# Kernel optimization log

Measured on AMD Instinct MI355X. Metric: run time of the kernel, lower is better.

The kernel has to match this reference:

```python
import jax, jax.numpy as jnp
import numpy as np

N = 100000      # nodes
E = 1600000     # edges (before self-loops)
FIN = 128       # in_channels
HID = 16        # hidden_channels
H = 8           # heads (layer 1)
OUT = 64        # out_channels
LN_EPS = 1e-5


def setup_inputs() -> dict:
    key = jax.random.key(0)
    ks = jax.random.split(key, 24)
    def p(i, shape):
        return jax.random.normal(ks[i], shape, dtype=jnp.float32) * 0.05
    return {
        "x": jax.random.normal(ks[0], (N, FIN), dtype=jnp.float32),
        "edge_index": jax.random.randint(ks[1], (2, E), 0, N, dtype=jnp.int32),
        # GATv2 layer 1: in -> H*HID, concat
        "Wl1": p(2, (FIN, H * HID)), "bl1": p(3, (H * HID,)),
        "Wr1": p(4, (FIN, H * HID)), "br1": p(5, (H * HID,)),
        "att1": p(6, (H, HID)), "bias1": p(7, (H * HID,)),
        # GATv2 layer 2: H*HID -> HID, heads=1
        "Wl2": p(8, (H * HID, HID)), "bl2": p(9, (HID,)),
        "Wr2": p(10, (H * HID, HID)), "br2": p(11, (HID,)),
        "att2": p(12, (1, HID)), "bias2": p(13, (HID,)),
        # LayerNorms
        "ln1_g": jnp.ones((H * HID,), jnp.float32), "ln1_b": jnp.zeros((H * HID,), jnp.float32),
        "ln2_g": jnp.ones((HID,), jnp.float32), "ln2_b": jnp.zeros((HID,), jnp.float32),
        # residual / skip / output linears
        "res1_W": p(14, (FIN, H * HID)), "res1_b": p(15, (H * HID,)),
        "res2_W": p(16, (H * HID, HID)), "res2_b": p(17, (HID,)),
        "skip_W": p(18, (H * HID, HID)), "skip_b": p(19, (HID,)),
        "out_W": p(20, (HID, OUT)), "out_b": p(21, (OUT,)),
    }


def _layernorm(x, g, b):
    mu = jnp.mean(x, axis=-1, keepdims=True)
    var = jnp.mean((x - mu) ** 2, axis=-1, keepdims=True)
    return (x - mu) * jax.lax.rsqrt(var + LN_EPS) * g + b


def _gatv2(x, src, dst, Wl, bl, Wr, br, att, bias, concat):
    # PyG GATv2Conv (share_weights=False, eval mode): message from src j to dst i
    Hh, C = att.shape
    n = x.shape[0]
    xl = (x @ Wl + bl).reshape(n, Hh, C)   # source-side transform
    xr = (x @ Wr + br).reshape(n, Hh, C)   # target-side transform
    m = xl[src] + xr[dst]                  # [E, H, C]
    e = jax.nn.leaky_relu(m, 0.2)
    alpha = jnp.einsum('ehc,hc->eh', e, att)          # [E, H]
    amax = jax.ops.segment_max(alpha, dst, num_segments=n)
    alpha = jnp.exp(alpha - amax[dst])
    denom = jax.ops.segment_sum(alpha, dst, num_segments=n)
    alpha = alpha / (denom[dst] + 1e-16)
    out = jax.ops.segment_sum(xl[src] * alpha[:, :, None], dst, num_segments=n)  # [N, H, C]
    out = out.reshape(n, Hh * C) if concat else out.mean(axis=1)
    return out + bias


def reference(x, edge_index, Wl1, bl1, Wr1, br1, att1, bias1,
              Wl2, bl2, Wr2, br2, att2, bias2,
              ln1_g, ln1_b, ln2_g, ln2_b,
              res1_W, res1_b, res2_W, res2_b, skip_W, skip_b, out_W, out_b):
    n = x.shape[0]
    loops = jnp.arange(n, dtype=edge_index.dtype)
    src = jnp.concatenate([edge_index[0], loops])
    dst = jnp.concatenate([edge_index[1], loops])

    h = _gatv2(x, src, dst, Wl1, bl1, Wr1, br1, att1, bias1, concat=True)
    h = _layernorm(h, ln1_g, ln1_b)
    h = h + (x @ res1_W + res1_b)
    h = jax.nn.elu(h)            # dropout off in eval

    skip_in = h
    h2 = _gatv2(h, src, dst, Wl2, bl2, Wr2, br2, att2, bias2, concat=False)
    h2 = _layernorm(h2, ln2_g, ln2_b)
    h2 = h2 + (skip_in @ res2_W + res2_b)
    h2 = jax.nn.elu(h2)
    h2 = h2 + (skip_in @ skip_W + skip_b)
    return h2 @ out_W + out_b
```

## Files before the change

### kernel.cpp

```cpp
#include <hip/hip_runtime.h>

typedef __attribute__((ext_vector_type(8))) short bf16x8;
typedef __attribute__((ext_vector_type(4))) float f32x4;

__device__ __forceinline__ float bf2f(ushort u) {
  union { uint i; float f; } v; v.i = ((uint)u) << 16; return v.f;
}
__device__ __forceinline__ ushort f2bf(float f) {
  union { float f; uint i; } v; v.f = f;
  uint r = (v.i + 0x7FFFu + ((v.i >> 16) & 1u)) >> 16;
  return (ushort)r;
}
__device__ __forceinline__ float blo(uint u) { return __builtin_bit_cast(float, u << 16); }
__device__ __forceinline__ float bhi(uint u) { return __builtin_bit_cast(float, u & 0xffff0000u); }

template <int CTRL>
__device__ __forceinline__ float dppadd(float x) {
  union { float f; int i; } a, b;
  a.f = x;
  b.i = __builtin_amdgcn_update_dpp(0, a.i, CTRL, 0xF, 0xF, true);
  return a.f + b.f;
}
#define DPP_X1 0xB1
#define DPP_X2 0x4E
#define DPP_X7 0x141
#define DPP_XF 0x140


__global__ __launch_bounds__(256) void k_init(
    const float* __restrict__ x, ushort* __restrict__ XF,
    const float* __restrict__ Wl1, const float* __restrict__ bl1,
    const float* __restrict__ Wr1, const float* __restrict__ br1,
    const float* __restrict__ res1W, const float* __restrict__ res1b,
    const float* __restrict__ Wl2, const float* __restrict__ bl2,
    const float* __restrict__ Wr2, const float* __restrict__ br2,
    const float* __restrict__ res2W, const float* __restrict__ res2b,
    const float* __restrict__ skipW, const float* __restrict__ skipb,
    const float* __restrict__ att1, const float* __restrict__ att2,
    ushort* __restrict__ W1F, float* __restrict__ B1P,
    ushort* __restrict__ W2F, float* __restrict__ B2P,
    float* __restrict__ at6, float* __restrict__ at4, float* __restrict__ at2E,
    int* __restrict__ cnt, int N) {
  const float LOG2E = 1.4426950408889634f;
  int b = blockIdx.x, t = threadIdx.x;
  int CB = (N * 16 + 255) >> 8;
  if (b < 227) {
    int tid = b * 256 + t;
    if (tid < 49152) {
      int j = tid & 7, l = (tid >> 3) & 63, ktile = (tid >> 9) & 3, ct = tid >> 11;
      int k = ktile * 32 + ((l >> 4) << 3) + j;
      int n = ct * 16 + (l & 15);
      int sel = n >> 7, jj = n & 127;
      const float* s = sel == 0 ? Wl1 : sel == 1 ? Wr1 : res1W;
      W1F[tid] = f2bf(s[k * 128 + jj]);
    } else if (tid < 57344) {
      int u = tid - 49152;
      int j = u & 7, l = (u >> 3) & 63, ktile = (u >> 9) & 3, ct = u >> 11;
      int k = ktile * 32 + ((l >> 4) << 3) + j;
      int n = ct * 16 + (l & 15);
      int sel = n >> 4, jj = n & 15;
      const float* s = sel == 0 ? Wl2 : sel == 1 ? Wr2 : sel == 2 ? res2W : skipW;
      W2F[u] = f2bf(s[k * 16 + jj]);
    } else if (tid < 57728) {
      int n = tid - 57344;
      int sel = n >> 7, jj = n & 127;
      const float* sb = sel == 0 ? bl1 : sel == 1 ? br1 : res1b;
      B1P[n] = sb[jj];
    } else if (tid < 57792) {
      int n = tid - 57728;
      int sel = n >> 4, jj = n & 15;
      const float* sb = sel == 0 ? bl2 : sel == 1 ? br2 : sel == 2 ? res2b : skipb;
      B2P[n] = sb[jj];
    } else if (tid < 57920) {
      int n = tid - 57792;
      at6[n] = att1[n] * 0.6f * LOG2E;
    } else if (tid < 58048) {
      int n = tid - 57920;
      at4[n] = att1[n] * 0.4f * LOG2E;
    } else if (tid < 58064) {
      int n = tid - 58048;
      at2E[n] = att2[n] * LOG2E;
    }
  } else if (b < 227 + CB) {
    int t2 = (b - 227) * 256 + t;
    if (t2 < N * 16) {
      int m = t2 >> 4, k8 = t2 & 15;
      const float* src = x + (size_t)m * 128 + k8 * 8;
      float4 f0 = *(const float4*)src;
      float4 f1 = *(const float4*)(src + 4);
      uint4 o;
      o.x = f2bf(f0.x) | ((uint)f2bf(f0.y) << 16);
      o.y = f2bf(f0.z) | ((uint)f2bf(f0.w) << 16);
      o.z = f2bf(f1.x) | ((uint)f2bf(f1.y) << 16);
      o.w = f2bf(f1.z) | ((uint)f2bf(f1.w) << 16);
      size_t off = ((size_t)(((m >> 4) * 4 + (k8 >> 2)) * 64) + (m & 15) + ((k8 & 3) << 4)) * 8;
      *(uint4*)(XF + off) = o;
    }
  } else {
    int idx = (b - 227 - CB) * 256 + t;
    if (idx < N) cnt[idx] = 0;
  }
}


__global__ __launch_bounds__(256) void k_hist(const int* __restrict__ ei, int* __restrict__ cnt, int E) {
  int e4 = (blockIdx.x * 256 + threadIdx.x) * 4;
  if (e4 + 3 < E) {
    int4 d = *(const int4*)&ei[E + e4];
    atomicAdd(&cnt[d.x], 1); atomicAdd(&cnt[d.y], 1);
    atomicAdd(&cnt[d.z], 1); atomicAdd(&cnt[d.w], 1);
  } else {
    for (int e = e4; e < E; ++e) atomicAdd(&cnt[ei[E + e]], 1);
  }
}


__global__ __launch_bounds__(256) void k_scan1(const int* __restrict__ cnt, int* __restrict__ partial, int n) {
  int i = blockIdx.x * 256 + threadIdx.x;
  int v = (i < n) ? cnt[i] : 0;
  #pragma unroll
  for (int m = 1; m < 64; m <<= 1) v += __shfl_xor(v, m);
  __shared__ int sm[4];
  if ((threadIdx.x & 63) == 0) sm[threadIdx.x >> 6] = v;
  __syncthreads();
  if (threadIdx.x == 0) partial[blockIdx.x] = sm[0] + sm[1] + sm[2] + sm[3];
}


__global__ __launch_bounds__(256) void k_scan3lb(const int* __restrict__ cnt, const int* __restrict__ partial,
                                                 int* __restrict__ rowptr, int* __restrict__ cursor, int n) {
  int t = threadIdx.x;
  int b = blockIdx.x;
  int acc = 0;
  for (int j = t; j < b; j += 256) acc += partial[j];
  #pragma unroll
  for (int m = 1; m < 64; m <<= 1) acc += __shfl_xor(acc, m);
  __shared__ int sm[4];
  if ((t & 63) == 0) sm[t >> 6] = acc;
  __syncthreads();
  int base = sm[0] + sm[1] + sm[2] + sm[3];
  __shared__ int buf[2][256];
  int i = b * 256 + t;
  int v = (i < n) ? cnt[i] : 0;
  buf[0][t] = v;
  __syncthreads();
  int cur = 0;
  for (int off = 1; off < 256; off <<= 1) {
    int x = buf[cur][t];
    if (t >= off) x += buf[cur][t - off];
    buf[cur ^ 1][t] = x;
    __syncthreads();
    cur ^= 1;
  }
  if (i < n) {
    int incl = buf[cur][t];
    int rp = base + incl - v;
    rowptr[i] = rp;
    cursor[i] = rp;
    if (i == n - 1) rowptr[n] = base + incl;
  }
}


__global__ __launch_bounds__(256) void k_scatgemm(
    const int* __restrict__ ei, int* __restrict__ cursor, int* __restrict__ ssrc, int E, int NS, int nScat,
    const ushort* __restrict__ AF, const ushort* __restrict__ WF, const float* __restrict__ bias,
    ushort* __restrict__ O0, ushort* __restrict__ O1, ushort* __restrict__ O2,
    int M, int nblk) {
  int b = blockIdx.x;
  int t = threadIdx.x;
  if (b < nScat) {
    int base = b * 2048;
    int src[8], dst[8];
    #pragma unroll
    for (int j = 0; j < 8; ++j) {
      int idx = base + j * 256 + t;
      bool ok = idx < E;
      src[j] = ok ? ei[idx] : 0;
      dst[j] = ok ? ei[E + idx] : -1;
    }
    for (int s = 0; s < NS; ++s) {
      #pragma unroll
      for (int j = 0; j < 8; ++j) {
        if ((dst[j] >> 13) == s) {
          int pos = atomicAdd(&cursor[dst[j]], 1);
          ssrc[pos] = src[j];
        }
      }
    }
  } else {
    int bb = b - nScat;
    int by = bb / nblk;
    int bx = bb - by * nblk;
    int w = t >> 6, l = t & 63;
    int m0 = bx * 64;
    int c0 = by * 64 + w * 16;
    int ct = c0 >> 4;
    f32x4 acc[4] = {};
    #pragma unroll
    for (int kt = 0; kt < 4; ++kt) {
      bf16x8 bfr = *(const bf16x8*)(WF + ((size_t)((ct * 4 + kt) * 64 + l)) * 8);
      #pragma unroll
      for (int rt = 0; rt < 4; ++rt) {
        bf16x8 a = *(const bf16x8*)(AF + ((size_t)((bx * 16 + rt * 4 + kt) * 64 + l)) * 8);
        acc[rt] = __builtin_amdgcn_mfma_f32_16x16x32_bf16(a, bfr, acc[rt], 0, 0, 0);
      }
    }
    int col = c0 + (l & 15);
    int arr = col >> 7;
    ushort* O = arr == 0 ? O0 : arr == 1 ? O1 : O2;
    int lcol = col & 127;
    float bv = bias[col];
    int rbase = m0 + ((l >> 4) << 2);
    #pragma unroll
    for (int rt = 0; rt < 4; ++rt) {
      #pragma unroll
      for (int r = 0; r < 4; ++r) {
        int m = rbase + rt * 16 + r;
        if (m < M) O[(size_t)m * 128 + lcol] = f2bf(acc[rt][r] + bv);
      }
    }
  }
}


__global__ __launch_bounds__(256) void k_mfma2(
    const ushort* __restrict__ AF, const ushort* __restrict__ WF,
    const float* __restrict__ bias,
    ushort* __restrict__ O0, ushort* __restrict__ O1,
    ushort* __restrict__ O2, ushort* __restrict__ O3, int M) {
  int w = threadIdx.x >> 6, l = threadIdx.x & 63;
  int m0 = blockIdx.x * 64;
  int c0 = w * 16;
  int ct = c0 >> 4;
  f32x4 acc[4] = {};
  #pragma unroll
  for (int kt = 0; kt < 4; ++kt) {
    bf16x8 b = *(const bf16x8*)(WF + ((size_t)((ct * 4 + kt) * 64 + l)) * 8);
    #pragma unroll
    for (int rt = 0; rt < 4; ++rt) {
      bf16x8 a = *(const bf16x8*)(AF + ((size_t)((blockIdx.x * 16 + rt * 4 + kt) * 64 + l)) * 8);
      acc[rt] = __builtin_amdgcn_mfma_f32_16x16x32_bf16(a, b, acc[rt], 0, 0, 0);
    }
  }
  int col = c0 + (l & 15);
  int arr = col >> 4;
  ushort* O = arr == 0 ? O0 : arr == 1 ? O1 : arr == 2 ? O2 : O3;
  int lcol = col & 15;
  float bv = bias[col];
  int rbase = m0 + ((l >> 4) << 2);
  #pragma unroll
  for (int rt = 0; rt < 4; ++rt) {
    #pragma unroll
    for (int r = 0; r < 4; ++r) {
      int m = rbase + rt * 16 + r;
      if (m < M) O[(size_t)m * 16 + lcol] = f2bf(acc[rt][r] + bv);
    }
  }
}


#define EDGE1B(u, MASKHI)                                              \
  {                                                                    \
    float v0 = blo((u).x), v1 = bhi((u).x);                            \
    float v2 = blo((u).y), v3 = bhi((u).y);                            \
    float m0 = v0 + xr0, m1 = v1 + xr1, m2 = v2 + xr2, m3 = v3 + xr3;  \
    float d = a6.x * m0 + a4.x * __builtin_fabsf(m0);                  \
    d += a6.y * m1; d += a4.y * __builtin_fabsf(m1);                   \
    d += a6.z * m2; d += a4.z * __builtin_fabsf(m2);                   \
    d += a6.w * m3; d += a4.w * __builtin_fabsf(m3);                   \
    d = dppadd<DPP_X1>(d);                                             \
    d = dppadd<DPP_X2>(d);                                             \
    float p = __builtin_amdgcn_exp2f(d);                               \
    if (MASKHI) p = hi ? 0.f : p;                                      \
    acc0 += p * v0; acc1 += p * v1; acc2 += p * v2; acc3 += p * v3;    \
    den += p;                                                          \
  }

__global__ __launch_bounds__(256) void k_gat1(
    const ushort* __restrict__ XLG, const ushort* __restrict__ XR,
    const ushort* __restrict__ RE,
    const float* __restrict__ at6, const float* __restrict__ at4,
    const float* __restrict__ bias1,
    const float* __restrict__ g1, const float* __restrict__ b1,
    const int* __restrict__ rowptr, const int* __restrict__ ssrc,
    ushort* __restrict__ HF, int n) {
  int lane = threadIdx.x & 63;
  int i = blockIdx.x * 4 + (threadIdx.x >> 6);
  if (i >= n) return;
  int l32 = lane & 31;
  bool hi = lane >= 32;
  int fb = l32 * 4;
  size_t rowb = (size_t)i << 8;
  uint2 uxr = *(const uint2*)((const char*)XR + rowb + (fb << 1));
  float xr0 = blo(uxr.x), xr1 = bhi(uxr.x), xr2 = blo(uxr.y), xr3 = bhi(uxr.y);
  float4 a6 = *(const float4*)&at6[fb];
  float4 a4 = *(const float4*)&at4[fb];
  float acc0 = 0.f, acc1 = 0.f, acc2 = 0.f, acc3 = 0.f, den = 0.f;
  {
    uint2 us = *(const uint2*)((const char*)XLG + rowb + (fb << 1));
    EDGE1B(us, true);
  }
  int e0 = __builtin_amdgcn_readfirstlane(rowptr[i]);
  int e1 = __builtin_amdgcn_readfirstlane(rowptr[i + 1]);
  for (int base = e0; base < e1; base += 64) {
    int cnt = e1 - base; if (cnt > 64) cnt = 64;
    int sidx = ssrc[base + (lane < cnt ? lane : cnt - 1)];
    int j = 0;
    for (; j + 4 <= cnt; j += 4) {
      int s0 = __builtin_amdgcn_readlane(sidx, j);
      int s1 = __builtin_amdgcn_readlane(sidx, j + 1);
      int s2 = __builtin_amdgcn_readlane(sidx, j + 2);
      int s3 = __builtin_amdgcn_readlane(sidx, j + 3);
      int rA = hi ? s1 : s0;
      int rB = hi ? s3 : s2;
      uint2 uA = *(const uint2*)((const char*)XLG + ((size_t)(uint)rA << 8) + (fb << 1));
      uint2 uB = *(const uint2*)((const char*)XLG + ((size_t)(uint)rB << 8) + (fb << 1));
      EDGE1B(uA, false);
      EDGE1B(uB, false);
    }
    for (; j + 2 <= cnt; j += 2) {
      int s0 = __builtin_amdgcn_readlane(sidx, j);
      int s1 = __builtin_amdgcn_readlane(sidx, j + 1);
      int r = hi ? s1 : s0;
      uint2 u = *(const uint2*)((const char*)XLG + ((size_t)(uint)r << 8) + (fb << 1));
      EDGE1B(u, false);
    }
    if (j < cnt) {
      int s0 = __builtin_amdgcn_readlane(sidx, j);
      uint2 u = *(const uint2*)((const char*)XLG + ((size_t)(uint)s0 << 8) + (fb << 1));
      EDGE1B(u, true);
    }
  }
  acc0 += __shfl_xor(acc0, 32);
  acc1 += __shfl_xor(acc1, 32);
  acc2 += __shfl_xor(acc2, 32);
  acc3 += __shfl_xor(acc3, 32);
  den  += __shfl_xor(den, 32);
  float inv = 1.f / (den + 1e-16f);
  float4 bv = *(const float4*)&bias1[fb];
  float o0 = acc0 * inv + bv.x, o1 = acc1 * inv + bv.y;
  float o2 = acc2 * inv + bv.z, o3 = acc3 * inv + bv.w;
  float s = o0 + o1 + o2 + o3;
  #pragma unroll
  for (int m = 1; m < 32; m <<= 1) s += __shfl_xor(s, m);
  float mu = s * (1.f / 128.f);
  float d0 = o0 - mu, d1 = o1 - mu, d2 = o2 - mu, d3 = o3 - mu;
  float q = d0 * d0 + d1 * d1 + d2 * d2 + d3 * d3;
  #pragma unroll
  for (int m = 1; m < 32; m <<= 1) q += __shfl_xor(q, m);
  float rstd = rsqrtf(q * (1.f / 128.f) + 1e-5f);
  float4 gg = *(const float4*)&g1[fb];
  float4 bb = *(const float4*)&b1[fb];
  uint2 ur = *(const uint2*)((const char*)RE + rowb + (fb << 1));
  float r0 = blo(ur.x), r1 = bhi(ur.x), r2 = blo(ur.y), r3 = bhi(ur.y);
  float y0 = d0 * rstd * gg.x + bb.x + r0;
  float y1 = d1 * rstd * gg.y + bb.y + r1;
  float y2 = d2 * rstd * gg.z + bb.z + r2;
  float y3 = d3 * rstd * gg.w + bb.w + r3;
  y0 = y0 > 0.f ? y0 : __expf(y0) - 1.f;
  y1 = y1 > 0.f ? y1 : __expf(y1) - 1.f;
  y2 = y2 > 0.f ? y2 : __expf(y2) - 1.f;
  y3 = y3 > 0.f ? y3 : __expf(y3) - 1.f;
  if (!hi) {
    int k8 = l32 >> 1;
    size_t slot = ((size_t)(i >> 4) * 4 + (k8 >> 2)) * 64 + (i & 15) + ((k8 & 3) << 4);
    uint2 o;
    o.x = (uint)f2bf(y0) | ((uint)f2bf(y1) << 16);
    o.y = (uint)f2bf(y2) | ((uint)f2bf(y3) << 16);
    *(uint2*)(HF + slot * 8 + (l32 & 1) * 4) = o;
  }
}


#define EDGE2V(v)                                            \
  {                                                          \
    float m = (v) + xr;                                      \
    float ta = a2 * m;                                       \
    float tb = a2 * __builtin_fabsf(m);                      \
    float tt = 0.6f * ta + 0.4f * tb;                        \
    tt = dppadd<DPP_X1>(tt);                                 \
    tt = dppadd<DPP_X2>(tt);                                 \
    tt = dppadd<DPP_X7>(tt);                                 \
    tt = dppadd<DPP_XF>(tt);                                 \
    float p = __builtin_amdgcn_exp2f(tt);                    \
    acc += p * (v); den += p;                                \
  }

__global__ __launch_bounds__(256) void k_gat2(
    const ushort* __restrict__ XG, const ushort* __restrict__ XRr,
    const ushort* __restrict__ XE, const ushort* __restrict__ XS,
    const float* __restrict__ at2E, const float* __restrict__ bias2,
    const float* __restrict__ g2, const float* __restrict__ b2,
    const int* __restrict__ rowptr, const int* __restrict__ ssrc,
    const float* __restrict__ outW, const float* __restrict__ outB,
    float* __restrict__ Out, int n) {
  __shared__ float sW[1024];
  __shared__ float sB[64];
  int t = threadIdx.x;
  for (int idx = t; idx < 1024; idx += 256) sW[idx] = outW[idx];
  if (t < 64) sB[t] = outB[t];
  __syncthreads();
  int c = t & 15;
  int i = blockIdx.x * 16 + (t >> 4);
  if (i >= n) return;
  size_t ib = (size_t)i << 4;
  float xl = bf2f(XG[ib + c]), xr = bf2f(XRr[ib + c]);
  float resv = bf2f(XE[ib + c]), skipv = bf2f(XS[ib + c]);
  float a2 = at2E[c];
  float acc = 0.f, den = 0.f;
  EDGE2V(xl);
  int e0 = rowptr[i], e1 = rowptr[i + 1];
  int e = e0;
  for (; e + 4 <= e1; e += 4) {
    int s0 = ssrc[e], s1 = ssrc[e + 1], s2 = ssrc[e + 2], s3 = ssrc[e + 3];
    float v0 = bf2f(XG[((size_t)(uint)s0 << 4) + c]);
    float v1 = bf2f(XG[((size_t)(uint)s1 << 4) + c]);
    float v2 = bf2f(XG[((size_t)(uint)s2 << 4) + c]);
    float v3 = bf2f(XG[((size_t)(uint)s3 << 4) + c]);
    EDGE2V(v0); EDGE2V(v1); EDGE2V(v2); EDGE2V(v3);
  }
  for (; e < e1; ++e) {
    int s = ssrc[e];
    float v = bf2f(XG[((size_t)(uint)s << 4) + c]);
    EDGE2V(v);
  }
  float o = acc / (den + 1e-16f) + bias2[c];
  float s = o;
  s = dppadd<DPP_X1>(s); s = dppadd<DPP_X2>(s); s = dppadd<DPP_X7>(s); s = dppadd<DPP_XF>(s);
  float mu = s * (1.f / 16.f);
  float d = o - mu;
  float q = d * d;
  q = dppadd<DPP_X1>(q); q = dppadd<DPP_X2>(q); q = dppadd<DPP_X7>(q); q = dppadd<DPP_XF>(q);
  float rstd = rsqrtf(q * (1.f / 16.f) + 1e-5f);
  float y = d * rstd * g2[c] + b2[c] + resv;
  y = y > 0.f ? y : __expf(y) - 1.f;
  y += skipv;
  float a0 = sB[c * 4 + 0], a1 = sB[c * 4 + 1], ao2 = sB[c * 4 + 2], a3 = sB[c * 4 + 3];
  #pragma unroll
  for (int cc = 0; cc < 16; ++cc) {
    float h = __shfl(y, cc, 16);
    a0 += h * sW[cc * 64 + c * 4 + 0];
    a1 += h * sW[cc * 64 + c * 4 + 1];
    ao2 += h * sW[cc * 64 + c * 4 + 2];
    a3 += h * sW[cc * 64 + c * 4 + 3];
  }
  *(float4*)&Out[(size_t)i * 64 + c * 4] = make_float4(a0, a1, ao2, a3);
}


extern "C" void kernel_launch(void* const* d_in, const int* in_sizes, int n_in,
                              void* d_out, int out_size, void* d_ws, size_t ws_size,
                              hipStream_t stream) {
  const float* x     = (const float*)d_in[0];
  const int*   ei    = (const int*)d_in[1];
  const float* Wl1   = (const float*)d_in[2];
  const float* bl1   = (const float*)d_in[3];
  const float* Wr1   = (const float*)d_in[4];
  const float* br1   = (const float*)d_in[5];
  const float* att1  = (const float*)d_in[6];
  const float* bias1 = (const float*)d_in[7];
  const float* Wl2   = (const float*)d_in[8];
  const float* bl2   = (const float*)d_in[9];
  const float* Wr2   = (const float*)d_in[10];
  const float* br2   = (const float*)d_in[11];
  const float* att2  = (const float*)d_in[12];
  const float* bias2 = (const float*)d_in[13];
  const float* ln1g  = (const float*)d_in[14];
  const float* ln1b  = (const float*)d_in[15];
  const float* ln2g  = (const float*)d_in[16];
  const float* ln2b  = (const float*)d_in[17];
  const float* res1W = (const float*)d_in[18];
  const float* res1b = (const float*)d_in[19];
  const float* res2W = (const float*)d_in[20];
  const float* res2b = (const float*)d_in[21];
  const float* skipW = (const float*)d_in[22];
  const float* skipb = (const float*)d_in[23];
  const float* outW  = (const float*)d_in[24];
  const float* outb  = (const float*)d_in[25];
  int N = in_sizes[0] / 128;
  int E = in_sizes[1] / 2;
  float* out = (float*)d_out;

  int nblk = (N + 63) / 64;
  int ngrp = nblk * 4;

  ushort* XF   = (ushort*)d_ws;
  ushort* XLG  = XF + (size_t)ngrp * 2048;
  ushort* XR1  = XLG + (size_t)N * 128;
  ushort* RE1  = XR1 + (size_t)N * 128;
  ushort* HF   = RE1 + (size_t)N * 128;
  ushort* XG2  = HF + (size_t)ngrp * 2048;
  ushort* X2R  = XG2 + (size_t)N * 16;
  ushort* X2E  = X2R + (size_t)N * 16;
  ushort* X2S  = X2E + (size_t)N * 16;
  ushort* W1F  = X2S + (size_t)N * 16;
  ushort* W2F  = W1F + 49152;
  float*  B1P  = (float*)(W2F + 8192);
  float*  B2P  = B1P + 384;
  float*  at6  = B2P + 64;
  float*  at4  = at6 + 128;
  float*  at2E = at4 + 128;
  int* cnt     = (int*)(at2E + 16);
  int* cursor  = cnt + N;
  int* rowptr  = cursor + N;
  int* ssrc    = rowptr + N + 1;
  int* partial = ssrc + E;

  int nbS = (N + 255) / 256;
  int CB  = (N * 16 + 255) / 256;
  int NS  = ((N - 1) >> 13) + 1;
  int nScat = (E + 2047) / 2048;

  k_init<<<227 + CB + nbS, 256, 0, stream>>>(x, XF, Wl1, bl1, Wr1, br1, res1W, res1b,
                                             Wl2, bl2, Wr2, br2, res2W, res2b, skipW, skipb,
                                             att1, att2, W1F, B1P, W2F, B2P, at6, at4, at2E,
                                             cnt, N);
  k_hist<<<(E + 1023) / 1024, 256, 0, stream>>>(ei, cnt, E);
  k_scan1<<<nbS, 256, 0, stream>>>(cnt, partial, N);
  k_scan3lb<<<nbS, 256, 0, stream>>>(cnt, partial, rowptr, cursor, N);
  k_scatgemm<<<nScat + nblk * 6, 256, 0, stream>>>(ei, cursor, ssrc, E, NS, nScat,
                                                   XF, W1F, B1P, XLG, XR1, RE1, N, nblk);
  k_gat1<<<(N + 3) / 4, 256, 0, stream>>>(XLG, XR1, RE1, at6, at4, bias1, ln1g, ln1b,
                                          rowptr, ssrc, HF, N);
  k_mfma2<<<nblk, 256, 0, stream>>>(HF, W2F, B2P, XG2, X2R, X2E, X2S, N);
  k_gat2<<<(N + 15) / 16, 256, 0, stream>>>(XG2, X2R, X2E, X2S, at2E, bias2, ln2g, ln2b,
                                            rowptr, ssrc, outW, outb, out, N);
}
```

Before: 459.0 us.

## Fuse x bf16 conversion into layer-1 GEMM and split scatter from GEMM

Drops the separate bf16 pre-pack of x in the init kernel. The new GEMM kernel reads fp32 x directly, converts it in registers, and computes all 384 output columns per 64-row block so x is read once. Outputs are staged through LDS and written back as coalesced 16-byte stores instead of scattered 2-byte stores. The edge scatter moves to its own kernel, which gives up the overlap it had with the GEMM inside one combined launch and adds a large LDS footprint that may reduce occupancy.

```diff
diff --git a/kernel.cpp b/kernel.cpp
--- a/kernel.cpp
+++ b/kernel.cpp
@@ -28,7 +28,6 @@
 
 
 __global__ __launch_bounds__(256) void k_init(
-    const float* __restrict__ x, ushort* __restrict__ XF,
     const float* __restrict__ Wl1, const float* __restrict__ bl1,
     const float* __restrict__ Wr1, const float* __restrict__ br1,
     const float* __restrict__ res1W, const float* __restrict__ res1b,
@@ -43,7 +42,6 @@
     int* __restrict__ cnt, int N) {
   const float LOG2E = 1.4426950408889634f;
   int b = blockIdx.x, t = threadIdx.x;
-  int CB = (N * 16 + 255) >> 8;
   if (b < 227) {
     int tid = b * 256 + t;
     if (tid < 49152) {
@@ -81,23 +79,8 @@
       int n = tid - 58048;
       at2E[n] = att2[n] * LOG2E;
     }
-  } else if (b < 227 + CB) {
-    int t2 = (b - 227) * 256 + t;
-    if (t2 < N * 16) {
-      int m = t2 >> 4, k8 = t2 & 15;
-      const float* src = x + (size_t)m * 128 + k8 * 8;
-      float4 f0 = *(const float4*)src;
-      float4 f1 = *(const float4*)(src + 4);
-      uint4 o;
-      o.x = f2bf(f0.x) | ((uint)f2bf(f0.y) << 16);
-      o.y = f2bf(f0.z) | ((uint)f2bf(f0.w) << 16);
-      o.z = f2bf(f1.x) | ((uint)f2bf(f1.y) << 16);
-      o.w = f2bf(f1.z) | ((uint)f2bf(f1.w) << 16);
-      size_t off = ((size_t)(((m >> 4) * 4 + (k8 >> 2)) * 64) + (m & 15) + ((k8 & 3) << 4)) * 8;
-      *(uint4*)(XF + off) = o;
-    }
   } else {
-    int idx = (b - 227 - CB) * 256 + t;
+    int idx = (b - 227) * 256 + t;
     if (idx < N) cnt[idx] = 0;
   }
 }
@@ -162,62 +145,89 @@
 }
 
 
-__global__ __launch_bounds__(256) void k_scatgemm(
-    const int* __restrict__ ei, int* __restrict__ cursor, int* __restrict__ ssrc, int E, int NS, int nScat,
-    const ushort* __restrict__ AF, const ushort* __restrict__ WF, const float* __restrict__ bias,
+__global__ __launch_bounds__(256) void k_scatter(const int* __restrict__ ei, int* __restrict__ cursor,
+                                                 int* __restrict__ ssrc, int E, int NS) {
+  int t = threadIdx.x;
+  int base = blockIdx.x * 2048;
+  int src[8], dst[8];
+  #pragma unroll
+  for (int j = 0; j < 8; ++j) {
+    int idx = base + j * 256 + t;
+    bool ok = idx < E;
+    src[j] = ok ? ei[idx] : 0;
+    dst[j] = ok ? ei[E + idx] : -1;
+  }
+  for (int s = 0; s < NS; ++s) {
+    #pragma unroll
+    for (int j = 0; j < 8; ++j) {
+      if ((dst[j] >> 13) == s) {
+        int pos = atomicAdd(&cursor[dst[j]], 1);
+        ssrc[pos] = src[j];
+      }
+    }
+  }
+}
+
+
+__global__ __launch_bounds__(256) void k_gemm1(
+    const float* __restrict__ x, const ushort* __restrict__ WF,
+    const float* __restrict__ bias,
     ushort* __restrict__ O0, ushort* __restrict__ O1, ushort* __restrict__ O2,
-    int M, int nblk) {
-  int b = blockIdx.x;
-  int t = threadIdx.x;
-  if (b < nScat) {
-    int base = b * 2048;
-    int src[8], dst[8];
-    #pragma unroll
-    for (int j = 0; j < 8; ++j) {
-      int idx = base + j * 256 + t;
-      bool ok = idx < E;
-      src[j] = ok ? ei[idx] : 0;
-      dst[j] = ok ? ei[E + idx] : -1;
-    }
-    for (int s = 0; s < NS; ++s) {
+    int M) {
+  __shared__ ushort LT[64 * 392];
+  int t = threadIdx.x, w = t >> 6, l = t & 63;
+  int m0 = blockIdx.x * 64;
+  int rql = l & 15, kq = l >> 4;
+  bf16x8 afr[16];
+  #pragma unroll
+  for (int kt = 0; kt < 4; ++kt) {
+    #pragma unroll
+    for (int rt = 0; rt < 4; ++rt) {
+      int m = m0 + rt * 16 + rql;
+      uint4 o = make_uint4(0, 0, 0, 0);
+      if (m < M) {
+        const float* src = x + (size_t)m * 128 + kt * 32 + kq * 8;
+        float4 f0 = *(const float4*)src;
+        float4 f1 = *(const float4*)(src + 4);
+        o.x = f2bf(f0.x) | ((uint)f2bf(f0.y) << 16);
+        o.y = f2bf(f0.z) | ((uint)f2bf(f0.w) << 16);
+        o.z = f2bf(f1.x) | ((uint)f2bf(f1.y) << 16);
+        o.w = f2bf(f1.z) | ((uint)f2bf(f1.w) << 16);
+      }
+      afr[kt * 4 + rt] = __builtin_bit_cast(bf16x8, o);
+    }
+  }
+  #pragma unroll
+  for (int ct6 = 0; ct6 < 6; ++ct6) {
+    int ct = w * 6 + ct6;
+    int col = ct * 16 + rql;
+    float bv = bias[col];
+    f32x4 acc[4] = {};
+    #pragma unroll
+    for (int kt = 0; kt < 4; ++kt) {
+      bf16x8 b = *(const bf16x8*)(WF + ((size_t)((ct * 4 + kt) * 64 + l)) * 8);
       #pragma unroll
-      for (int j = 0; j < 8; ++j) {
-        if ((dst[j] >> 13) == s) {
-          int pos = atomicAdd(&cursor[dst[j]], 1);
-          ssrc[pos] = src[j];
-        }
-      }
-    }
-  } else {
-    int bb = b - nScat;
-    int by = bb / nblk;
-    int bx = bb - by * nblk;
-    int w = t >> 6, l = t & 63;
-    int m0 = bx * 64;
-    int c0 = by * 64 + w * 16;
-    int ct = c0 >> 4;
-    f32x4 acc[4] = {};
-    #pragma unroll
-    for (int kt = 0; kt < 4; ++kt) {
-      bf16x8 bfr = *(const bf16x8*)(WF + ((size_t)((ct * 4 + kt) * 64 + l)) * 8);
+      for (int rt = 0; rt < 4; ++rt)
+        acc[rt] = __builtin_amdgcn_mfma_f32_16x16x32_bf16(afr[kt * 4 + rt], b, acc[rt], 0, 0, 0);
+    }
+    #pragma unroll
+    for (int rt = 0; rt < 4; ++rt)
       #pragma unroll
-      for (int rt = 0; rt < 4; ++rt) {
-        bf16x8 a = *(const bf16x8*)(AF + ((size_t)((bx * 16 + rt * 4 + kt) * 64 + l)) * 8);
-        acc[rt] = __builtin_amdgcn_mfma_f32_16x16x32_bf16(a, bfr, acc[rt], 0, 0, 0);
-      }
-    }
-    int col = c0 + (l & 15);
-    int arr = col >> 7;
-    ushort* O = arr == 0 ? O0 : arr == 1 ? O1 : O2;
-    int lcol = col & 127;
-    float bv = bias[col];
-    int rbase = m0 + ((l >> 4) << 2);
-    #pragma unroll
-    for (int rt = 0; rt < 4; ++rt) {
-      #pragma unroll
-      for (int r = 0; r < 4; ++r) {
-        int m = rbase + rt * 16 + r;
-        if (m < M) O[(size_t)m * 128 + lcol] = f2bf(acc[rt][r] + bv);
+      for (int r = 0; r < 4; ++r)
+        LT[(rt * 16 + kq * 4 + r) * 392 + col] = f2bf(acc[rt][r] + bv);
+  }
+  __syncthreads();
+  #pragma unroll
+  for (int a = 0; a < 3; ++a) {
+    ushort* O = a == 0 ? O0 : a == 1 ? O1 : O2;
+    #pragma unroll
+    for (int it = 0; it < 4; ++it) {
+      int idx = it * 256 + t;
+      int row = idx >> 4, seg = idx & 15;
+      int m = m0 + row;
+      if (m < M) {
+        uint4 v = *(const uint4*)&LT[row * 392 + a * 128 + seg * 8];
+        *(uint4*)&O[(size_t)m * 128 + seg * 8] = v;
       }
     }
   }
@@ -485,8 +495,7 @@
   int nblk = (N + 63) / 64;
   int ngrp = nblk * 4;
 
-  ushort* XF   = (ushort*)d_ws;
-  ushort* XLG  = XF + (size_t)ngrp * 2048;
+  ushort* XLG  = (ushort*)d_ws;
   ushort* XR1  = XLG + (size_t)N * 128;
   ushort* RE1  = XR1 + (size_t)N * 128;
   ushort* HF   = RE1 + (size_t)N * 128;
@@ -508,19 +517,18 @@
   int* partial = ssrc + E;
 
   int nbS = (N + 255) / 256;
-  int CB  = (N * 16 + 255) / 256;
   int NS  = ((N - 1) >> 13) + 1;
   int nScat = (E + 2047) / 2048;
 
-  k_init<<<227 + CB + nbS, 256, 0, stream>>>(x, XF, Wl1, bl1, Wr1, br1, res1W, res1b,
-                                             Wl2, bl2, Wr2, br2, res2W, res2b, skipW, skipb,
-                                             att1, att2, W1F, B1P, W2F, B2P, at6, at4, at2E,
-                                             cnt, N);
+  k_init<<<227 + nbS, 256, 0, stream>>>(Wl1, bl1, Wr1, br1, res1W, res1b,
+                                        Wl2, bl2, Wr2, br2, res2W, res2b, skipW, skipb,
+                                        att1, att2, W1F, B1P, W2F, B2P, at6, at4, at2E,
+                                        cnt, N);
   k_hist<<<(E + 1023) / 1024, 256, 0, stream>>>(ei, cnt, E);
   k_scan1<<<nbS, 256, 0, stream>>>(cnt, partial, N);
   k_scan3lb<<<nbS, 256, 0, stream>>>(cnt, partial, rowptr, cursor, N);
-  k_scatgemm<<<nScat + nblk * 6, 256, 0, stream>>>(ei, cursor, ssrc, E, NS, nScat,
-                                                   XF, W1F, B1P, XLG, XR1, RE1, N, nblk);
+  k_scatter<<<nScat, 256, 0, stream>>>(ei, cursor, ssrc, E, NS);
+  k_gemm1<<<nblk, 256, 0, stream>>>(x, W1F, B1P, XLG, XR1, RE1, N);
   k_gat1<<<(N + 3) / 4, 256, 0, stream>>>(XLG, XR1, RE1, at6, at4, bias1, ln1g, ln1b,
                                           rowptr, ssrc, HF, N);
   k_mfma2<<<nblk, 256, 0, stream>>>(HF, W2F, B2P, XG2, X2R, X2E, X2S, N);
```

After: 472.9 us. 1.03x slower.
